# Kernel optimization log

Hardware: AMD Instinct MI355X
Metric: run time of the kernel (lower is better)

## Reference

```python
import jax, jax.numpy as jnp
import numpy as np

D_MODEL = 1024
N_HEADS = 16
D_HEAD = D_MODEL // N_HEADS
WINDOW = 256
SCALE = D_HEAD ** -0.5


def setup_inputs() -> dict:
    key = jax.random.key(0)
    k1, k2, k3, k4, k5 = jax.random.split(key, 5)
    B, S = 2, 2048
    x = jax.random.normal(k1, (B, S, D_MODEL), dtype=jnp.float32)
    s = 0.02
    Wqkv = jax.random.normal(k2, (D_MODEL, 3 * D_MODEL), dtype=jnp.float32) * s
    bqkv = jnp.zeros((3 * D_MODEL,), dtype=jnp.float32)
    Wout = jax.random.normal(k3, (D_MODEL, D_MODEL), dtype=jnp.float32) * s
    bout = jnp.zeros((D_MODEL,), dtype=jnp.float32)
    return {"x": x, "Wqkv": Wqkv, "bqkv": bqkv, "Wout": Wout, "bout": bout}


def reference(x, Wqkv, bqkv, Wout, bout):
    B, S, D = x.shape
    qkv = x @ Wqkv + bqkv                       # (B, S, 3D)
    q, k, v = jnp.split(qkv, 3, axis=-1)
    # (B, H, S, d)
    q = q.reshape(B, S, N_HEADS, D_HEAD).transpose(0, 2, 1, 3)
    k = k.reshape(B, S, N_HEADS, D_HEAD).transpose(0, 2, 1, 3)
    v = v.reshape(B, S, N_HEADS, D_HEAD).transpose(0, 2, 1, 3)
    scores = jnp.einsum('bhqd,bhkd->bhqk', q, k) * SCALE
    # windowed causal mask: allow j <= i and j >= i - WINDOW (inclusive),
    # matching torch code where mask[i, :i-window_size] = 0 for i >= window_size
    i = jnp.arange(S)[:, None]
    j = jnp.arange(S)[None, :]
    allowed = (j <= i) & (j >= i - WINDOW)      # (S, S)
    scores = jnp.where(allowed[None, None], scores, -jnp.inf)
    attn = jax.nn.softmax(scores, axis=-1)      # dropout=0 / eval mode
    out = jnp.einsum('bhqk,bhkd->bhqd', attn, v)
    out = out.transpose(0, 2, 1, 3).reshape(B, S, D)
    return out @ Wout + bout
```

## Files before the change

kernel.cpp:

```cpp
#include <hip/hip_runtime.h>
#include <stdint.h>


typedef __attribute__((ext_vector_type(8))) short bf16x8;
typedef __attribute__((ext_vector_type(4))) float f32x4;
typedef __attribute__((ext_vector_type(4))) unsigned int u32x4;
typedef __attribute__((ext_vector_type(4))) unsigned short u16x4;

#define DEV static __device__ __forceinline__

#define SC2 0.18033688011112042f

DEV unsigned short f2bf(float f) {
  unsigned int u = __builtin_bit_cast(unsigned int, f);
  u += 0x7fffu + ((u >> 16) & 1u);
  return (unsigned short)(u >> 16);
}

DEV void gload_lds16(const void* g, void* l) {
  __builtin_amdgcn_global_load_lds((const __attribute__((address_space(1))) void*)g,
                                   (__attribute__((address_space(3))) void*)l,
                                   16, 0, 0);
}

__global__ __launch_bounds__(256) void k_prep(const float* __restrict__ x,
                                              const float* __restrict__ Wqkv,
                                              const float* __restrict__ Wout,
                                              const float* __restrict__ bqkv,
                                              unsigned short* __restrict__ xb,
                                              unsigned short* __restrict__ wqT,
                                              unsigned short* __restrict__ woT,
                                              float* __restrict__ bqkv_s) {
  __shared__ float t[32][33];
  const int bid = blockIdx.x, tid = threadIdx.x;
  if (bid < 4096) {
    int i = bid * 256 + tid;
    f32x4 v = ((const f32x4*)x)[i];
    u16x4 o;
    o[0] = f2bf(v[0]); o[1] = f2bf(v[1]); o[2] = f2bf(v[2]); o[3] = f2bf(v[3]);
    ((u16x4*)xb)[i] = o;
    return;
  }
  if (bid >= 8192) {
    int i = (bid - 8192) * 256 + tid;
    if (i < 3072) bqkv_s[i] = bqkv[i] * (i < 1024 ? SC2 : 1.0f);
    return;
  }
  const float* in;
  unsigned short* out;
  int N, K, n0, k0;
  float wscale = 1.0f;
  if (bid < 7168) {
    int tt = bid - 4096;
    in = Wqkv; out = wqT; N = 3072; K = 1024;
    n0 = (tt % 96) * 32; k0 = (tt / 96) * 32;
    if (n0 < 1024) wscale = SC2;
  } else {
    int tt = bid - 7168;
    in = Wout; out = woT; N = 1024; K = 1024;
    n0 = (tt % 32) * 32; k0 = (tt / 32) * 32;
  }
  const int tx = tid & 31, ty = tid >> 5;
#pragma unroll
  for (int i = 0; i < 4; ++i)
    t[ty + i * 8][tx] = in[(size_t)(k0 + ty + i * 8) * N + n0 + tx];
  __syncthreads();
#pragma unroll
  for (int i = 0; i < 4; ++i)
    out[(size_t)(n0 + ty + i * 8) * K + k0 + tx] = f2bf(t[tx][ty + i * 8] * wscale);
}

template <int BN, bool F32OUT, bool FUSE_VT>
__global__ __launch_bounds__(512) void k_gemmbig(const unsigned short* __restrict__ A,
                                                 const unsigned short* __restrict__ Bt,
                                                 const float* __restrict__ bias,
                                                 void* __restrict__ Cout,
                                                 unsigned short* __restrict__ vT,
                                                 int M, int N, int K) {
  constexpr int NI = BN / 32;
  constexpr int ACH = 32;
  constexpr int NCH = ACH + BN / 8;
  constexpr int ASZ = 256 * 64;
  constexpr int BSZ = BN * 64;
  extern __shared__ unsigned short lds[];
  const int tid = threadIdx.x;
  const int lane = tid & 63, wid = tid >> 6;
  const int wr = wid >> 1, wc = wid & 1;
  const int g = lane >> 4, li = lane & 15;
  const int m0 = blockIdx.y * 256, n0 = blockIdx.x * BN;

  f32x4 acc[4][NI] = {};
  const int nkt = K >> 6;
  const int r8 = lane >> 3, sp = lane & 7;

  auto Abuf = [&](int i) { return lds + i * ASZ; };
  auto Bbuf = [&](int i) { return lds + 2 * ASZ + i * BSZ; };

  auto stage = [&](int bufi, int kt) {
#pragma unroll
    for (int c = wid; c < NCH; c += 8) {
      if (c < ACH) {
        int row = c * 8 + r8;
        int sl = sp ^ (row & 7);
        gload_lds16(A + (size_t)(m0 + row) * K + kt * 64 + sl * 8,
                    Abuf(bufi) + c * 512);
      } else {
        int cc = c - ACH;
        int row = cc * 8 + r8;
        int sl = sp ^ (row & 7);
        gload_lds16(Bt + (size_t)(n0 + row) * K + kt * 64 + sl * 8,
                    Bbuf(bufi) + cc * 512);
      }
    }
  };

  stage(0, 0);
  for (int kt = 0; kt < nkt; ++kt) {
    __syncthreads();
    if (kt + 1 < nkt) stage((kt + 1) & 1, kt + 1);
    const unsigned short* Ac = Abuf(kt & 1);
    const unsigned short* Bc = Bbuf(kt & 1);
#pragma unroll
    for (int h = 0; h < 2; ++h) {
      bf16x8 af[4], bfr[NI];
#pragma unroll
      for (int mi = 0; mi < 4; ++mi) {
        const int r = wr * 64 + mi * 16 + li;
        const int slot = (g + h * 4) ^ (r & 7);
        af[mi] = *(const bf16x8*)&Ac[r * 64 + slot * 8];
      }
#pragma unroll
      for (int ni = 0; ni < NI; ++ni) {
        const int r = wc * (BN / 2) + ni * 16 + li;
        const int slot = (g + h * 4) ^ (r & 7);
        bfr[ni] = *(const bf16x8*)&Bc[r * 64 + slot * 8];
      }
#pragma unroll
      for (int mi = 0; mi < 4; ++mi)
#pragma unroll
        for (int ni = 0; ni < NI; ++ni)
          acc[mi][ni] = __builtin_amdgcn_mfma_f32_16x16x32_bf16(af[mi], bfr[ni],
                                                                acc[mi][ni], 0, 0, 0);
    }
  }

  float bv[NI];
#pragma unroll
  for (int ni = 0; ni < NI; ++ni) bv[ni] = bias[n0 + wc * (BN / 2) + ni * 16 + li];
#pragma unroll
  for (int mi = 0; mi < 4; ++mi) {
#pragma unroll
    for (int ni = 0; ni < NI; ++ni) {
      const int col = n0 + wc * (BN / 2) + ni * 16 + li;
      const int row0 = m0 + wr * 64 + mi * 16 + g * 4;
      float v0 = acc[mi][ni][0] + bv[ni];
      float v1 = acc[mi][ni][1] + bv[ni];
      float v2 = acc[mi][ni][2] + bv[ni];
      float v3 = acc[mi][ni][3] + bv[ni];
      if (F32OUT) {
        float* C = (float*)Cout;
        C[(size_t)(row0 + 0) * N + col] = v0;
        C[(size_t)(row0 + 1) * N + col] = v1;
        C[(size_t)(row0 + 2) * N + col] = v2;
        C[(size_t)(row0 + 3) * N + col] = v3;
      } else {
        unsigned short* C = (unsigned short*)Cout;
        C[(size_t)(row0 + 0) * N + col] = f2bf(v0);
        C[(size_t)(row0 + 1) * N + col] = f2bf(v1);
        C[(size_t)(row0 + 2) * N + col] = f2bf(v2);
        C[(size_t)(row0 + 3) * N + col] = f2bf(v3);
      }
      if (FUSE_VT && col >= 2048) {
        const int b = row0 >> 11;
        const int s = row0 & 2047;
        u16x4 vv;
        vv[0] = f2bf(v0); vv[1] = f2bf(v1); vv[2] = f2bf(v2); vv[3] = f2bf(v3);
        *(u16x4*)&vT[(size_t)(b * 1024 + col - 2048) * 2048 + s] = vv;
      }
    }
  }
}

__global__ __launch_bounds__(512) void k_attn5(const unsigned short* __restrict__ qkv,
                                               const unsigned short* __restrict__ vT,
                                               unsigned short* __restrict__ attn) {
  __shared__ unsigned short Ks[2][64 * 64];
  __shared__ unsigned short Vs[2][64 * 64];
  __shared__ unsigned short Ps[128 * 88];
  const int tid = threadIdx.x, lane = tid & 63, wid = tid >> 6;
  const int g = lane >> 4, li = lane & 15;
  const int bh = blockIdx.y, b = bh >> 4, h = bh & 15;
  const int bx = blockIdx.x, q0 = bx * 128;
  const size_t rs = 3072;
  const unsigned short* qb = qkv + (size_t)b * 2048 * rs + h * 64;
  const unsigned short* kb = qb + 1024;
  const unsigned short* vb = vT + (size_t)bh * 64 * 2048;

  const int qrow = wid * 16 + li;
  const bf16x8 qf0 = *(const bf16x8*)(qb + (size_t)(q0 + qrow) * rs + (g << 3));
  const bf16x8 qf1 = *(const bf16x8*)(qb + (size_t)(q0 + qrow) * rs + 32 + (g << 3));

  const int tf_blk = (bx >= 2) ? 0 : (4 - 2 * bx);
  const int tfw = (wid >= 4) ? 1 : 0;
  const int tlw = tfw + 4;

  auto stage = [&](int bufi, int t) {
    const int j0 = q0 - 256 + t * 64;
    const int row = wid * 8 + (lane >> 3);
    const int sl = (lane & 7) ^ (row & 7);
    gload_lds16(kb + (size_t)(j0 + row) * rs + sl * 8, &Ks[bufi][wid * 512]);
    gload_lds16(vb + (size_t)row * 2048 + j0 + sl * 8, &Vs[bufi][wid * 512]);
  };

  f32x4 o[4] = {};
  float l_part[4] = {0.f, 0.f, 0.f, 0.f};

  stage(0, tf_blk);
  int cur = 0;
  for (int t = tf_blk; t < 6; ++t) {
    if (t + 1 < 6) {
      stage(cur ^ 1, t + 1);
      asm volatile("s_waitcnt vmcnt(2)" ::: "memory");
    } else {
      asm volatile("s_waitcnt vmcnt(0)" ::: "memory");
    }
    __builtin_amdgcn_sched_barrier(0);
    __builtin_amdgcn_s_barrier();
    __builtin_amdgcn_sched_barrier(0);

    if (t >= tfw && t <= tlw) {
      const unsigned short* Kc = Ks[cur];
      const unsigned short* Vc = Vs[cur];

      f32x4 s[4];
#pragma unroll
      for (int ni = 0; ni < 4; ++ni) {
        const int kr = ni * 16 + li;
        const int sw = (kr & 7);
        bf16x8 kf0 = *(const bf16x8*)&Kc[kr * 64 + ((g ^ sw) << 3)];
        bf16x8 kf1 = *(const bf16x8*)&Kc[kr * 64 + (((4 + g) ^ sw) << 3)];
        f32x4 z = {};
        z = __builtin_amdgcn_mfma_f32_16x16x32_bf16(qf0, kf0, z, 0, 0, 0);
        z = __builtin_amdgcn_mfma_f32_16x16x32_bf16(qf1, kf1, z, 0, 0, 0);
        s[ni] = z;
      }
      const int rt = (wid & 3) * 16 + g * 4;
#pragma unroll
      for (int ni = 0; ni < 4; ++ni) {
        int ct = ni * 16 + li;
#pragma unroll
        for (int reg = 0; reg < 4; ++reg) {
          float sv = s[ni][reg];
          if (t == tlw && ct > rt + reg) sv = -3e30f;
          if (t == tfw && ct < rt + reg) sv = -3e30f;
          s[ni][reg] = sv;
        }
      }
#pragma unroll
      for (int reg = 0; reg < 4; ++reg) {
        float ps = 0.f;
#pragma unroll
        for (int ni = 0; ni < 4; ++ni) {
          float p = __builtin_exp2f(s[ni][reg] - 16.0f);
          ps += p;
          Ps[(wid * 16 + g * 4 + reg) * 88 + ni * 16 + li] = f2bf(p);
        }
        l_part[reg] += ps;
      }
      asm volatile("s_waitcnt lgkmcnt(0)" ::: "memory");
      __builtin_amdgcn_sched_barrier(0);
      const bf16x8 pf0 = *(const bf16x8*)&Ps[(wid * 16 + li) * 88 + (g << 3)];
      const bf16x8 pf1 = *(const bf16x8*)&Ps[(wid * 16 + li) * 88 + 32 + (g << 3)];
#pragma unroll
      for (int ni = 0; ni < 4; ++ni) {
        const int dr = ni * 16 + li;
        const int sw = (dr & 7);
        bf16x8 vf0 = *(const bf16x8*)&Vc[dr * 64 + ((g ^ sw) << 3)];
        bf16x8 vf1 = *(const bf16x8*)&Vc[dr * 64 + (((4 + g) ^ sw) << 3)];
        o[ni] = __builtin_amdgcn_mfma_f32_16x16x32_bf16(pf0, vf0, o[ni], 0, 0, 0);
        o[ni] = __builtin_amdgcn_mfma_f32_16x16x32_bf16(pf1, vf1, o[ni], 0, 0, 0);
      }
    }
    __builtin_amdgcn_sched_barrier(0);
    __builtin_amdgcn_s_barrier();
    cur ^= 1;
  }

  float inv[4];
#pragma unroll
  for (int reg = 0; reg < 4; ++reg) {
    float L = l_part[reg];
    L += __shfl_xor(L, 1, 64);
    L += __shfl_xor(L, 2, 64);
    L += __shfl_xor(L, 4, 64);
    L += __shfl_xor(L, 8, 64);
    inv[reg] = 1.f / L;
  }
#pragma unroll
  for (int ni = 0; ni < 4; ++ni) {
#pragma unroll
    for (int reg = 0; reg < 4; ++reg) {
      size_t row = (size_t)b * 2048 + q0 + wid * 16 + g * 4 + reg;
      attn[row * 1024 + h * 64 + ni * 16 + li] = f2bf(o[ni][reg] * inv[reg]);
    }
  }
}

extern "C" void kernel_launch(void* const* d_in, const int* in_sizes, int n_in,
                              void* d_out, int out_size, void* d_ws, size_t ws_size,
                              hipStream_t stream) {
  const float* x    = (const float*)d_in[0];
  const float* Wqkv = (const float*)d_in[1];
  const float* bqkv = (const float*)d_in[2];
  const float* Wout = (const float*)d_in[3];
  const float* bout = (const float*)d_in[4];
  float* out = (float*)d_out;

  uint8_t* ws = (uint8_t*)d_ws;
  unsigned short* xb    = (unsigned short*)(ws);
  unsigned short* wqT   = (unsigned short*)(ws +  8388608);
  unsigned short* woT   = (unsigned short*)(ws + 14680064);
  unsigned short* qkvb  = (unsigned short*)(ws + 16777216);
  unsigned short* attnb = (unsigned short*)(ws + 41943040);
  unsigned short* vTb   = (unsigned short*)(ws + 50331648);
  float*          bqs   = (float*)(ws + 58720256);

  (void)hipFuncSetAttribute((const void*)k_gemmbig<192, false, true>,
                            hipFuncAttributeMaxDynamicSharedMemorySize, 114688);
  (void)hipFuncSetAttribute((const void*)k_gemmbig<64, true, false>,
                            hipFuncAttributeMaxDynamicSharedMemorySize, 81920);

  k_prep<<<8204, 256, 0, stream>>>(x, Wqkv, Wout, bqkv, xb, wqT, woT, bqs);
  k_gemmbig<192, false, true><<<dim3(3072 / 192, 4096 / 256), 512, 114688, stream>>>(
      xb, wqT, bqs, qkvb, vTb, 4096, 3072, 1024);
  k_attn5<<<dim3(2048 / 128, 32), 512, 0, stream>>>(qkvb, vTb, attnb);
  k_gemmbig<64, true, false><<<dim3(1024 / 64, 4096 / 256), 512, 81920, stream>>>(
      attnb, woT, bout, out, nullptr, 4096, 1024, 1024);
}
```

Before: 81.45 us.

## Fuse prep, QKV GEMM, attention and output GEMM into one persistent kernel

Replaces four kernel launches with a single persistent kernel of 256 blocks that runs each stage in turn, separated by atomic-counter grid barriers. Grid sizes are remapped so each block handles one GEMM tile or two attention units per stage. The goal is to remove launch overhead and the gaps between kernels. In exchange it relies on all 256 blocks being co-resident, otherwise the barrier spin deadlocks. It also loses the finer-grained scheduling of the separate kernels and adds a memset and barrier spin cost.

After: 160.2 us. 96.7% more time.

```diff
diff --git a/kernel.cpp b/kernel.cpp
--- a/kernel.cpp
+++ b/kernel.cpp
@@ -23,71 +23,36 @@
                                    16, 0, 0);
 }
 
-__global__ __launch_bounds__(256) void k_prep(const float* __restrict__ x,
-                                              const float* __restrict__ Wqkv,
-                                              const float* __restrict__ Wout,
-                                              const float* __restrict__ bqkv,
-                                              unsigned short* __restrict__ xb,
-                                              unsigned short* __restrict__ wqT,
-                                              unsigned short* __restrict__ woT,
-                                              float* __restrict__ bqkv_s) {
-  __shared__ float t[32][33];
-  const int bid = blockIdx.x, tid = threadIdx.x;
-  if (bid < 4096) {
-    int i = bid * 256 + tid;
-    f32x4 v = ((const f32x4*)x)[i];
-    u16x4 o;
-    o[0] = f2bf(v[0]); o[1] = f2bf(v[1]); o[2] = f2bf(v[2]); o[3] = f2bf(v[3]);
-    ((u16x4*)xb)[i] = o;
-    return;
-  }
-  if (bid >= 8192) {
-    int i = (bid - 8192) * 256 + tid;
-    if (i < 3072) bqkv_s[i] = bqkv[i] * (i < 1024 ? SC2 : 1.0f);
-    return;
-  }
-  const float* in;
-  unsigned short* out;
-  int N, K, n0, k0;
-  float wscale = 1.0f;
-  if (bid < 7168) {
-    int tt = bid - 4096;
-    in = Wqkv; out = wqT; N = 3072; K = 1024;
-    n0 = (tt % 96) * 32; k0 = (tt / 96) * 32;
-    if (n0 < 1024) wscale = SC2;
-  } else {
-    int tt = bid - 7168;
-    in = Wout; out = woT; N = 1024; K = 1024;
-    n0 = (tt % 32) * 32; k0 = (tt / 32) * 32;
-  }
-  const int tx = tid & 31, ty = tid >> 5;
-#pragma unroll
-  for (int i = 0; i < 4; ++i)
-    t[ty + i * 8][tx] = in[(size_t)(k0 + ty + i * 8) * N + n0 + tx];
+DEV void gridbar(unsigned int* c) {
   __syncthreads();
-#pragma unroll
-  for (int i = 0; i < 4; ++i)
-    out[(size_t)(n0 + ty + i * 8) * K + k0 + tx] = f2bf(t[tx][ty + i * 8] * wscale);
+  if (threadIdx.x == 0) {
+    __threadfence();
+    atomicAdd(c, 1u);
+    while (atomicAdd(c, 0u) < 256u) { __builtin_amdgcn_s_sleep(8); }
+    __threadfence();
+  }
+  __syncthreads();
 }
 
 template <int BN, bool F32OUT, bool FUSE_VT>
-__global__ __launch_bounds__(512) void k_gemmbig(const unsigned short* __restrict__ A,
-                                                 const unsigned short* __restrict__ Bt,
-                                                 const float* __restrict__ bias,
-                                                 void* __restrict__ Cout,
-                                                 unsigned short* __restrict__ vT,
-                                                 int M, int N, int K) {
+DEV void gemm_body(unsigned short* lds,
+                   const unsigned short* __restrict__ A,
+                   const unsigned short* __restrict__ Bt,
+                   const float* __restrict__ bias,
+                   void* __restrict__ Cout,
+                   unsigned short* __restrict__ vT,
+                   int N, int K) {
   constexpr int NI = BN / 32;
   constexpr int ACH = 32;
   constexpr int NCH = ACH + BN / 8;
   constexpr int ASZ = 256 * 64;
   constexpr int BSZ = BN * 64;
-  extern __shared__ unsigned short lds[];
   const int tid = threadIdx.x;
   const int lane = tid & 63, wid = tid >> 6;
   const int wr = wid >> 1, wc = wid & 1;
   const int g = lane >> 4, li = lane & 15;
-  const int m0 = blockIdx.y * 256, n0 = blockIdx.x * BN;
+  const int m0 = ((int)blockIdx.x >> 4) * 256;
+  const int n0 = ((int)blockIdx.x & 15) * BN;
 
   f32x4 acc[4][NI] = {};
   const int nkt = K >> 6;
@@ -143,6 +108,7 @@
                                                                 acc[mi][ni], 0, 0, 0);
     }
   }
+  __syncthreads();
 
   float bv[NI];
 #pragma unroll
@@ -152,7 +118,7 @@
 #pragma unroll
     for (int ni = 0; ni < NI; ++ni) {
       const int col = n0 + wc * (BN / 2) + ni * 16 + li;
-      const int row0 = m0 + wr * 64 + mi * 16 + g * 4;
+      const int row0 = ((int)blockIdx.x >> 4) * 256 + wr * 64 + mi * 16 + g * 4;
       float v0 = acc[mi][ni][0] + bv[ni];
       float v1 = acc[mi][ni][1] + bv[ni];
       float v2 = acc[mi][ni][2] + bv[ni];
@@ -181,129 +147,193 @@
   }
 }
 
-__global__ __launch_bounds__(512) void k_attn5(const unsigned short* __restrict__ qkv,
-                                               const unsigned short* __restrict__ vT,
-                                               unsigned short* __restrict__ attn) {
-  __shared__ unsigned short Ks[2][64 * 64];
-  __shared__ unsigned short Vs[2][64 * 64];
-  __shared__ unsigned short Ps[128 * 88];
-  const int tid = threadIdx.x, lane = tid & 63, wid = tid >> 6;
-  const int g = lane >> 4, li = lane & 15;
-  const int bh = blockIdx.y, b = bh >> 4, h = bh & 15;
-  const int bx = blockIdx.x, q0 = bx * 128;
-  const size_t rs = 3072;
-  const unsigned short* qb = qkv + (size_t)b * 2048 * rs + h * 64;
-  const unsigned short* kb = qb + 1024;
-  const unsigned short* vb = vT + (size_t)bh * 64 * 2048;
-
-  const int qrow = wid * 16 + li;
-  const bf16x8 qf0 = *(const bf16x8*)(qb + (size_t)(q0 + qrow) * rs + (g << 3));
-  const bf16x8 qf1 = *(const bf16x8*)(qb + (size_t)(q0 + qrow) * rs + 32 + (g << 3));
-
-  const int tf_blk = (bx >= 2) ? 0 : (4 - 2 * bx);
-  const int tfw = (wid >= 4) ? 1 : 0;
-  const int tlw = tfw + 4;
-
-  auto stage = [&](int bufi, int t) {
-    const int j0 = q0 - 256 + t * 64;
-    const int row = wid * 8 + (lane >> 3);
-    const int sl = (lane & 7) ^ (row & 7);
-    gload_lds16(kb + (size_t)(j0 + row) * rs + sl * 8, &Ks[bufi][wid * 512]);
-    gload_lds16(vb + (size_t)row * 2048 + j0 + sl * 8, &Vs[bufi][wid * 512]);
-  };
-
-  f32x4 o[4] = {};
-  float l_part[4] = {0.f, 0.f, 0.f, 0.f};
-
-  stage(0, tf_blk);
-  int cur = 0;
-  for (int t = tf_blk; t < 6; ++t) {
-    if (t + 1 < 6) {
-      stage(cur ^ 1, t + 1);
-      asm volatile("s_waitcnt vmcnt(2)" ::: "memory");
-    } else {
-      asm volatile("s_waitcnt vmcnt(0)" ::: "memory");
-    }
-    __builtin_amdgcn_sched_barrier(0);
-    __builtin_amdgcn_s_barrier();
-    __builtin_amdgcn_sched_barrier(0);
-
-    if (t >= tfw && t <= tlw) {
-      const unsigned short* Kc = Ks[cur];
-      const unsigned short* Vc = Vs[cur];
-
-      f32x4 s[4];
+__global__ __launch_bounds__(512) void k_mega(
+    const float* __restrict__ x, const float* __restrict__ Wqkv,
+    const float* __restrict__ Wout, const float* __restrict__ bqkv,
+    const float* __restrict__ bout,
+    unsigned short* __restrict__ xb, unsigned short* __restrict__ wqT,
+    unsigned short* __restrict__ woT, float* __restrict__ bqs,
+    unsigned short* __restrict__ qkvb, unsigned short* __restrict__ attnb,
+    unsigned short* __restrict__ vT, float* __restrict__ out,
+    unsigned int* __restrict__ bar) {
+  extern __shared__ unsigned short lds[];
+  const int tid = threadIdx.x;
+  const int bid = blockIdx.x;
+
+  for (int i = bid * 512 + tid; i < 1048576; i += 131072) {
+    f32x4 v = ((const f32x4*)x)[i];
+    u16x4 o;
+    o[0] = f2bf(v[0]); o[1] = f2bf(v[1]); o[2] = f2bf(v[2]); o[3] = f2bf(v[3]);
+    ((u16x4*)xb)[i] = o;
+  }
+  if (bid * 512 + tid < 3072) {
+    int i = bid * 512 + tid;
+    bqs[i] = bqkv[i] * (i < 1024 ? SC2 : 1.0f);
+  }
+  {
+    const int team = tid >> 8, ttid = tid & 255;
+    const int tx = ttid & 31, ty = ttid >> 5;
+    float* tt = (float*)lds + team * (32 * 33);
+    for (int tile = bid * 2 + team; tile < 4096; tile += 512) {
+      const float* in;
+      unsigned short* outp;
+      int N, K, n0, k0;
+      float wscale = 1.0f;
+      if (tile < 3072) {
+        in = Wqkv; outp = wqT; N = 3072; K = 1024;
+        n0 = (tile % 96) * 32; k0 = (tile / 96) * 32;
+        if (n0 < 1024) wscale = SC2;
+      } else {
+        int t2 = tile - 3072;
+        in = Wout; outp = woT; N = 1024; K = 1024;
+        n0 = (t2 % 32) * 32; k0 = (t2 / 32) * 32;
+      }
+#pragma unroll
+      for (int i = 0; i < 4; ++i)
+        tt[(ty + i * 8) * 33 + tx] = in[(size_t)(k0 + ty + i * 8) * N + n0 + tx];
+      __syncthreads();
+#pragma unroll
+      for (int i = 0; i < 4; ++i)
+        outp[(size_t)(n0 + ty + i * 8) * K + k0 + tx] =
+            f2bf(tt[tx * 33 + ty + i * 8] * wscale);
+      __syncthreads();
+    }
+  }
+  gridbar(bar + 0);
+
+  gemm_body<192, false, true>(lds, xb, wqT, bqs, qkvb, vT, 3072, 1024);
+  gridbar(bar + 1);
+
+  {
+    const int lane = tid & 63, wid = tid >> 6;
+    const int g = lane >> 4, li = lane & 15;
+    const size_t rs = 3072;
+    for (int u = 0; u < 2; ++u) {
+      const int unit = bid * 2 + u;
+      const int bx = unit & 15, bh = unit >> 4;
+      const int b = bh >> 4, h = bh & 15;
+      const int q0 = bx * 128;
+      const unsigned short* qb = qkvb + (size_t)b * 2048 * rs + h * 64;
+      const unsigned short* kb = qb + 1024;
+      const unsigned short* vb = vT + (size_t)bh * 64 * 2048;
+
+      const int qrow = wid * 16 + li;
+      const bf16x8 qf0 = *(const bf16x8*)(qb + (size_t)(q0 + qrow) * rs + (g << 3));
+      const bf16x8 qf1 = *(const bf16x8*)(qb + (size_t)(q0 + qrow) * rs + 32 + (g << 3));
+
+      const int tf_blk = (bx >= 2) ? 0 : (4 - 2 * bx);
+      const int tfw = (wid >= 4) ? 1 : 0;
+      const int tlw = tfw + 4;
+
+      auto stage = [&](int bufi, int t) {
+        const int j0 = q0 - 256 + t * 64;
+        const int row = wid * 8 + (lane >> 3);
+        const int sl = (lane & 7) ^ (row & 7);
+        gload_lds16(kb + (size_t)(j0 + row) * rs + sl * 8,
+                    lds + bufi * 4096 + wid * 512);
+        gload_lds16(vb + (size_t)row * 2048 + j0 + sl * 8,
+                    lds + 8192 + bufi * 4096 + wid * 512);
+      };
+
+      f32x4 o[4] = {};
+      float l_part[4] = {0.f, 0.f, 0.f, 0.f};
+
+      __syncthreads();
+      stage(0, tf_blk);
+      int cur = 0;
+      for (int t = tf_blk; t < 6; ++t) {
+        if (t + 1 < 6) {
+          stage(cur ^ 1, t + 1);
+          asm volatile("s_waitcnt vmcnt(2)" ::: "memory");
+        } else {
+          asm volatile("s_waitcnt vmcnt(0)" ::: "memory");
+        }
+        __builtin_amdgcn_sched_barrier(0);
+        __builtin_amdgcn_s_barrier();
+        __builtin_amdgcn_sched_barrier(0);
+
+        if (t >= tfw && t <= tlw) {
+          const unsigned short* Kc = lds + cur * 4096;
+          const unsigned short* Vc = lds + 8192 + cur * 4096;
+          unsigned short* Ps = lds + 16384;
+
+          f32x4 s[4];
+#pragma unroll
+          for (int ni = 0; ni < 4; ++ni) {
+            const int kr = ni * 16 + li;
+            const int sw = (kr & 7);
+            bf16x8 kf0 = *(const bf16x8*)&Kc[kr * 64 + ((g ^ sw) << 3)];
+            bf16x8 kf1 = *(const bf16x8*)&Kc[kr * 64 + (((4 + g) ^ sw) << 3)];
+            f32x4 z = {};
+            z = __builtin_amdgcn_mfma_f32_16x16x32_bf16(qf0, kf0, z, 0, 0, 0);
+            z = __builtin_amdgcn_mfma_f32_16x16x32_bf16(qf1, kf1, z, 0, 0, 0);
+            s[ni] = z;
+          }
+          const int rt = (wid & 3) * 16 + g * 4;
+#pragma unroll
+          for (int ni = 0; ni < 4; ++ni) {
+            int ct = ni * 16 + li;
+#pragma unroll
+            for (int reg = 0; reg < 4; ++reg) {
+              float sv = s[ni][reg];
+              if (t == tlw && ct > rt + reg) sv = -3e30f;
+              if (t == tfw && ct < rt + reg) sv = -3e30f;
+              s[ni][reg] = sv;
+            }
+          }
+#pragma unroll
+          for (int reg = 0; reg < 4; ++reg) {
+            float ps = 0.f;
+#pragma unroll
+            for (int ni = 0; ni < 4; ++ni) {
+              float p = __builtin_exp2f(s[ni][reg] - 16.0f);
+              ps += p;
+              Ps[(wid * 16 + g * 4 + reg) * 88 + ni * 16 + li] = f2bf(p);
+            }
+            l_part[reg] += ps;
+          }
+          asm volatile("s_waitcnt lgkmcnt(0)" ::: "memory");
+          __builtin_amdgcn_sched_barrier(0);
+          const bf16x8 pf0 = *(const bf16x8*)&Ps[(wid * 16 + li) * 88 + (g << 3)];
+          const bf16x8 pf1 = *(const bf16x8*)&Ps[(wid * 16 + li) * 88 + 32 + (g << 3)];
+#pragma unroll
+          for (int ni = 0; ni < 4; ++ni) {
+            const int dr = ni * 16 + li;
+            const int sw = (dr & 7);
+            bf16x8 vf0 = *(const bf16x8*)&Vc[dr * 64 + ((g ^ sw) << 3)];
+            bf16x8 vf1 = *(const bf16x8*)&Vc[dr * 64 + (((4 + g) ^ sw) << 3)];
+            o[ni] = __builtin_amdgcn_mfma_f32_16x16x32_bf16(pf0, vf0, o[ni], 0, 0, 0);
+            o[ni] = __builtin_amdgcn_mfma_f32_16x16x32_bf16(pf1, vf1, o[ni], 0, 0, 0);
+          }
+        }
+        __builtin_amdgcn_sched_barrier(0);
+        __builtin_amdgcn_s_barrier();
+        cur ^= 1;
+      }
+
+      float inv[4];
+#pragma unroll
+      for (int reg = 0; reg < 4; ++reg) {
+        float L = l_part[reg];
+        L += __shfl_xor(L, 1, 64);
+        L += __shfl_xor(L, 2, 64);
+        L += __shfl_xor(L, 4, 64);
+        L += __shfl_xor(L, 8, 64);
+        inv[reg] = 1.f / L;
+      }
 #pragma unroll
       for (int ni = 0; ni < 4; ++ni) {
-        const int kr = ni * 16 + li;
-        const int sw = (kr & 7);
-        bf16x8 kf0 = *(const bf16x8*)&Kc[kr * 64 + ((g ^ sw) << 3)];
-        bf16x8 kf1 = *(const bf16x8*)&Kc[kr * 64 + (((4 + g) ^ sw) << 3)];
-        f32x4 z = {};
-        z = __builtin_amdgcn_mfma_f32_16x16x32_bf16(qf0, kf0, z, 0, 0, 0);
-        z = __builtin_amdgcn_mfma_f32_16x16x32_bf16(qf1, kf1, z, 0, 0, 0);
-        s[ni] = z;
-      }
-      const int rt = (wid & 3) * 16 + g * 4;
-#pragma unroll
-      for (int ni = 0; ni < 4; ++ni) {
-        int ct = ni * 16 + li;
 #pragma unroll
         for (int reg = 0; reg < 4; ++reg) {
-          float sv = s[ni][reg];
-          if (t == tlw && ct > rt + reg) sv = -3e30f;
-          if (t == tfw && ct < rt + reg) sv = -3e30f;
-          s[ni][reg] = sv;
+          size_t row = (size_t)b * 2048 + q0 + wid * 16 + g * 4 + reg;
+          attnb[row * 1024 + h * 64 + ni * 16 + li] = f2bf(o[ni][reg] * inv[reg]);
         }
       }
-#pragma unroll
-      for (int reg = 0; reg < 4; ++reg) {
-        float ps = 0.f;
-#pragma unroll
-        for (int ni = 0; ni < 4; ++ni) {
-          float p = __builtin_exp2f(s[ni][reg] - 16.0f);
-          ps += p;
-          Ps[(wid * 16 + g * 4 + reg) * 88 + ni * 16 + li] = f2bf(p);
-        }
-        l_part[reg] += ps;
-      }
-      asm volatile("s_waitcnt lgkmcnt(0)" ::: "memory");
-      __builtin_amdgcn_sched_barrier(0);
-      const bf16x8 pf0 = *(const bf16x8*)&Ps[(wid * 16 + li) * 88 + (g << 3)];
-      const bf16x8 pf1 = *(const bf16x8*)&Ps[(wid * 16 + li) * 88 + 32 + (g << 3)];
-#pragma unroll
-      for (int ni = 0; ni < 4; ++ni) {
-        const int dr = ni * 16 + li;
-        const int sw = (dr & 7);
-        bf16x8 vf0 = *(const bf16x8*)&Vc[dr * 64 + ((g ^ sw) << 3)];
-        bf16x8 vf1 = *(const bf16x8*)&Vc[dr * 64 + (((4 + g) ^ sw) << 3)];
-        o[ni] = __builtin_amdgcn_mfma_f32_16x16x32_bf16(pf0, vf0, o[ni], 0, 0, 0);
-        o[ni] = __builtin_amdgcn_mfma_f32_16x16x32_bf16(pf1, vf1, o[ni], 0, 0, 0);
-      }
-    }
-    __builtin_amdgcn_sched_barrier(0);
-    __builtin_amdgcn_s_barrier();
-    cur ^= 1;
-  }
-
-  float inv[4];
-#pragma unroll
-  for (int reg = 0; reg < 4; ++reg) {
-    float L = l_part[reg];
-    L += __shfl_xor(L, 1, 64);
-    L += __shfl_xor(L, 2, 64);
-    L += __shfl_xor(L, 4, 64);
-    L += __shfl_xor(L, 8, 64);
-    inv[reg] = 1.f / L;
-  }
-#pragma unroll
-  for (int ni = 0; ni < 4; ++ni) {
-#pragma unroll
-    for (int reg = 0; reg < 4; ++reg) {
-      size_t row = (size_t)b * 2048 + q0 + wid * 16 + g * 4 + reg;
-      attn[row * 1024 + h * 64 + ni * 16 + li] = f2bf(o[ni][reg] * inv[reg]);
-    }
-  }
+    }
+  }
+  gridbar(bar + 2);
+
+  gemm_body<64, true, false>(lds, attnb, woT, bout, out, nullptr, 1024, 1024);
 }
 
 extern "C" void kernel_launch(void* const* d_in, const int* in_sizes, int n_in,
@@ -324,16 +354,13 @@
   unsigned short* attnb = (unsigned short*)(ws + 41943040);
   unsigned short* vTb   = (unsigned short*)(ws + 50331648);
   float*          bqs   = (float*)(ws + 58720256);
-
-  (void)hipFuncSetAttribute((const void*)k_gemmbig<192, false, true>,
+  unsigned int*   bar   = (unsigned int*)(ws + 58736640);
+
+  (void)hipFuncSetAttribute((const void*)k_mega,
                             hipFuncAttributeMaxDynamicSharedMemorySize, 114688);
-  (void)hipFuncSetAttribute((const void*)k_gemmbig<64, true, false>,
-                            hipFuncAttributeMaxDynamicSharedMemorySize, 81920);
-
-  k_prep<<<8204, 256, 0, stream>>>(x, Wqkv, Wout, bqkv, xb, wqT, woT, bqs);
-  k_gemmbig<192, false, true><<<dim3(3072 / 192, 4096 / 256), 512, 114688, stream>>>(
-      xb, wqT, bqs, qkvb, vTb, 4096, 3072, 1024);
-  k_attn5<<<dim3(2048 / 128, 32), 512, 0, stream>>>(qkvb, vTb, attnb);
-  k_gemmbig<64, true, false><<<dim3(1024 / 64, 4096 / 256), 512, 81920, stream>>>(
-      attnb, woT, bout, out, nullptr, 4096, 1024, 1024);
-}
+  (void)hipMemsetAsync(bar, 0, 16, stream);
+
+  k_mega<<<256, 512, 114688, stream>>>(x, Wqkv, Wout, bqkv, bout,
+                                       xb, wqT, woT, bqs,
+                                       qkvb, attnb, vTb, out, bar);
+}
```
